# Optimization experiments

Measured on AMD Instinct MI355X. Metric: run time of the kernel, lower is better.

Reference implementation:

```python
import jax, jax.numpy as jnp
import numpy as np

N, E, IN_C, HID, OUT_C, L = 100000, 1600000, 128, 128, 128, 3
BN_EPS = 1e-5


def setup_inputs() -> dict:
    key = jax.random.key(0)
    ks = jax.random.split(key, 16)
    inp = {
        "x": jax.random.normal(ks[0], (N, IN_C), dtype=jnp.float32),
        "edge_index": jax.random.randint(ks[1], (2, E), 0, N, dtype=jnp.int64),
        "edge_attr": jax.random.normal(ks[2], (E, 1), dtype=jnp.float32),
        # input/output projections (math uses [in, out] layout)
        "lin0_w": jax.random.normal(ks[3], (IN_C, HID), dtype=jnp.float32) / np.sqrt(IN_C),
        "lin0_b": jnp.zeros((HID,), dtype=jnp.float32),
        "lin1_w": jax.random.normal(ks[4], (HID, OUT_C), dtype=jnp.float32) / np.sqrt(HID),
        "lin1_b": jnp.zeros((OUT_C,), dtype=jnp.float32),
        # stacked GCNConv weights/biases
        "conv_w": jax.random.normal(ks[5], (L, HID, HID), dtype=jnp.float32) / np.sqrt(HID),
        "conv_b": jnp.zeros((L, HID), dtype=jnp.float32),
        # BatchNorm1d (eval mode: running stats are buffers)
        "bn_gamma": jnp.ones((L, HID), dtype=jnp.float32),
        "bn_beta": jnp.zeros((L, HID), dtype=jnp.float32),
        "bn_mean": 0.1 * jax.random.normal(ks[6], (L, HID), dtype=jnp.float32),
        "bn_var": jax.random.uniform(ks[7], (L, HID), minval=0.5, maxval=1.5, dtype=jnp.float32),
    }
    return inp


def reference(x, edge_index, edge_attr, lin0_w, lin0_b, lin1_w, lin1_b,
              conv_w, conv_b, bn_gamma, bn_beta, bn_mean, bn_var):
    n = x.shape[0]
    # GCN normalization with self-loops (computed once; identical every layer)
    loops = jnp.arange(n, dtype=edge_index.dtype)
    src = jnp.concatenate([edge_index[0], loops])  # [E+N]
    dst = jnp.concatenate([edge_index[1], loops])  # [E+N]
    deg = jax.ops.segment_sum(jnp.ones_like(src, dtype=x.dtype), dst, num_segments=n)
    dinv = jnp.where(deg > 0, deg ** -0.5, 0.0)
    norm = dinv[src] * dinv[dst]  # [E+N]

    # input projection + relu (dropout p used in eval -> identity)
    h = jax.nn.relu(x @ lin0_w + lin0_b)

    for l in range(L):
        hw = h @ conv_w[l]                                         # [N, H]
        msg = hw[src] * norm[:, None]                              # [E+N, H]
        agg = jax.ops.segment_sum(msg, dst, num_segments=n) + conv_b[l]
        # BatchNorm1d (inference) + ReLU activation
        h = (agg - bn_mean[l]) * jax.lax.rsqrt(bn_var[l] + BN_EPS) * bn_gamma[l] + bn_beta[l]
        h = jax.nn.relu(h)

    out = h @ lin1_w + lin1_b
    return out
```

## Files before the change

kernel.cpp:

```cpp
#include <hip/hip_runtime.h>
#include <hip/hip_fp16.h>


#define HIDC 128
#define BN_EPS 1e-5f
#define DPB 256
#define NBK 512
#define BIN_CHUNK 8192

typedef short bf16x8 __attribute__((ext_vector_type(8)));
typedef float f32x4 __attribute__((ext_vector_type(4)));

__device__ __forceinline__ unsigned short f2bf_rn(float x) {
    unsigned int u = __float_as_uint(x);
    unsigned int r = u + 0x7fffu + ((u >> 16) & 1u);
    return (unsigned short)(r >> 16);
}
__device__ __forceinline__ float bf2f(unsigned short b) {
    return __uint_as_float(((unsigned int)b) << 16);
}


__global__ void detect64(const unsigned int* ei, int* flag) {
    if (threadIdx.x != 0 || blockIdx.x != 0) return;
    int is64 = 1;
    for (int i = 0; i < 64; ++i) {
        if (ei[2 * i + 1] != 0u) { is64 = 0; break; }
    }
    *flag = is64;
}

__global__ __launch_bounds__(256) void bucket_count(const void* __restrict__ ei,
                                                    const int* __restrict__ flag,
                                                    int* __restrict__ bkt, int e) {
    __shared__ int h[NBK];
    int t = threadIdx.x;
    for (int i = t; i < NBK; i += 256) h[i] = 0;
    __syncthreads();
    int base = blockIdx.x * BIN_CHUNK;
    int cnt = e - base;
    if (cnt > BIN_CHUNK) cnt = BIN_CHUNK;
    if (*flag) {
        const long long* pd = (const long long*)ei + e;
        for (int i = t; i < cnt; i += 256) atomicAdd(&h[((int)pd[base + i]) >> 8], 1);
    } else {
        const int* pd = (const int*)ei + e;
        for (int i = t; i < cnt; i += 256) atomicAdd(&h[pd[base + i] >> 8], 1);
    }
    __syncthreads();
    for (int i = t; i < NBK; i += 256) if (h[i]) atomicAdd(&bkt[i], h[i]);
}

__global__ void scan_buckets(const int* __restrict__ bkt, int* __restrict__ bbase,
                             int* __restrict__ bc, int* __restrict__ rowptr,
                             int n, int e, int nbk) {
    __shared__ int s[NBK];
    int t = threadIdx.x;
    int v = (t < nbk) ? bkt[t] : 0;
    s[t] = v;
    __syncthreads();
    for (int off = 1; off < NBK; off <<= 1) {
        int val = (t >= off) ? s[t - off] : 0;
        __syncthreads();
        s[t] += val;
        __syncthreads();
    }
    int excl = s[t] - v;
    bbase[t] = excl;
    bc[t] = excl;
    if (t == 0) rowptr[n] = e;
}

__global__ __launch_bounds__(256) void bin_pairs(const void* __restrict__ ei,
                                                 const int* __restrict__ flag,
                                                 int* __restrict__ bc,
                                                 int2* __restrict__ staged, int e) {
    __shared__ int hist[NBK];
    __shared__ int lstart[NBK];
    __shared__ int gbase[NBK];
    __shared__ int sdata[256];
    __shared__ int2 stage[BIN_CHUNK];

    int t = threadIdx.x;
    int base = blockIdx.x * BIN_CHUNK;
    int cnt = e - base;
    if (cnt > BIN_CHUNK) cnt = BIN_CHUNK;
    int is64 = *flag;

    for (int i = t; i < NBK; i += 256) hist[i] = 0;
    __syncthreads();
    if (is64) {
        const long long* pd = (const long long*)ei + e;
        for (int i = t; i < cnt; i += 256) atomicAdd(&hist[((int)pd[base + i]) >> 8], 1);
    } else {
        const int* pd = (const int*)ei + e;
        for (int i = t; i < cnt; i += 256) atomicAdd(&hist[pd[base + i] >> 8], 1);
    }
    __syncthreads();

    int a0 = hist[2 * t], a1 = hist[2 * t + 1];
    int s = a0 + a1;
    sdata[t] = s;
    __syncthreads();
    for (int off = 1; off < 256; off <<= 1) {
        int val = (t >= off) ? sdata[t - off] : 0;
        __syncthreads();
        sdata[t] += val;
        __syncthreads();
    }
    int excl = sdata[t] - s;
    lstart[2 * t] = excl;
    lstart[2 * t + 1] = excl + a0;
    if (a0 > 0) gbase[2 * t] = atomicAdd(&bc[2 * t], a0);
    if (a1 > 0) gbase[2 * t + 1] = atomicAdd(&bc[2 * t + 1], a1);
    hist[2 * t] = excl;
    hist[2 * t + 1] = excl + a0;
    __syncthreads();

    if (is64) {
        const long long* ps = (const long long*)ei;
        const long long* pd = ps + e;
        for (int i = t; i < cnt; i += 256) {
            int2 p = make_int2((int)ps[base + i], (int)pd[base + i]);
            int pos = atomicAdd(&hist[p.y >> 8], 1);
            stage[pos] = p;
        }
    } else {
        const int* ps = (const int*)ei;
        const int* pd = ps + e;
        for (int i = t; i < cnt; i += 256) {
            int2 p = make_int2(ps[base + i], pd[base + i]);
            int pos = atomicAdd(&hist[p.y >> 8], 1);
            stage[pos] = p;
        }
    }
    __syncthreads();

    for (int i = t; i < cnt; i += 256) {
        int2 p = stage[i];
        int b = p.y >> 8;
        staged[gbase[b] + (i - lstart[b])] = p;
    }
}

__global__ __launch_bounds__(256) void fill_bucket(const int2* __restrict__ staged,
                                                   const int* __restrict__ bbase,
                                                   float* __restrict__ dinv,
                                                   int* __restrict__ rowptr,
                                                   int* __restrict__ col, int n) {
    __shared__ int cnt[DPB];
    __shared__ int scn[DPB];
    int b = blockIdx.x;
    int t = threadIdx.x;
    int dstart = b * DPB;
    int ebeg = bbase[b], eend = bbase[b + 1];
    cnt[t] = 0;
    __syncthreads();
    for (int i = ebeg + t; i < eend; i += 256)
        atomicAdd(&cnt[staged[i].y - dstart], 1);
    __syncthreads();
    int my = cnt[t];
    scn[t] = my;
    __syncthreads();
    for (int off = 1; off < 256; off <<= 1) {
        int val = (t >= off) ? scn[t - off] : 0;
        __syncthreads();
        scn[t] += val;
        __syncthreads();
    }
    int excl = scn[t] - my;
    int v = dstart + t;
    if (v < n) {
        rowptr[v] = ebeg + excl;
        dinv[v] = rsqrtf((float)(my + 1));
    }
    cnt[t] = excl;
    __syncthreads();
    for (int i = ebeg + t; i < eend; i += 256) {
        int2 p = staged[i];
        int pos = atomicAdd(&cnt[p.y - dstart], 1);
        col[ebeg + pos] = p.x;
    }
}


__global__ __launch_bounds__(256) void pack_w(const float* __restrict__ lin0,
                                              const float* __restrict__ conv,
                                              const float* __restrict__ lin1,
                                              uint4* __restrict__ wf) {
    int tid = blockIdx.x * 256 + threadIdx.x;
    if (tid >= 5 * 2048) return;
    int mat = tid >> 11;
    int rem = tid & 2047;
    int ks = rem >> 9;
    int tt = (rem >> 6) & 7;
    int l = rem & 63;
    const float* W = (mat == 0) ? lin0 : (mat == 4) ? lin1 : conv + (size_t)(mat - 1) * 16384;
    int kbase = ks * 32 + (l >> 4) * 8;
    int c = tt * 16 + (l & 15);
    unsigned int hi[4], lo[4];
#pragma unroll
    for (int d = 0; d < 4; ++d) {
        float w0 = W[(kbase + 2 * d) * 128 + c];
        float w1 = W[(kbase + 2 * d + 1) * 128 + c];
        unsigned short h0 = f2bf_rn(w0), h1 = f2bf_rn(w1);
        unsigned short l0 = f2bf_rn(w0 - bf2f(h0)), l1 = f2bf_rn(w1 - bf2f(h1));
        hi[d] = (unsigned int)h0 | ((unsigned int)h1 << 16);
        lo[d] = (unsigned int)l0 | ((unsigned int)l1 << 16);
    }
    int rec = (ks * 8 + tt) * 64 + l;
    wf[(size_t)mat * 4096 + rec] = make_uint4(hi[0], hi[1], hi[2], hi[3]);
    wf[(size_t)mat * 4096 + 2048 + rec] = make_uint4(lo[0], lo[1], lo[2], lo[3]);
}


__global__ __launch_bounds__(512) void gemm_mfma(
    const float* __restrict__ A, const uint4* __restrict__ wf,
    const float* __restrict__ bias, const float* __restrict__ dinv,
    void* __restrict__ Cout, int M, int mode) {
    __shared__ uint4 WfL[4096];

    int t = threadIdx.x;
#pragma unroll
    for (int i = 0; i < 8; ++i) WfL[t + i * 512] = wf[t + i * 512];

    int wave = t >> 6, lane = t & 63;
    int lrow = lane & 15, lgrp = lane >> 4;
    int r0 = blockIdx.x * 128 + wave * 16;

    f32x4 acc[8];
#pragma unroll
    for (int i = 0; i < 8; ++i) acc[i] = (f32x4){0.f, 0.f, 0.f, 0.f};

    __syncthreads();

    int arow = r0 + lrow;
    if (arow >= M) arow = M - 1;
    const float* ap = A + (size_t)arow * 128 + lgrp * 8;

#pragma unroll
    for (int ks = 0; ks < 4; ++ks) {
        float4 v0 = *(const float4*)(ap + ks * 32);
        float4 v1 = *(const float4*)(ap + ks * 32 + 4);
        float av[8] = {v0.x, v0.y, v0.z, v0.w, v1.x, v1.y, v1.z, v1.w};
        bf16x8 ahi, alo;
#pragma unroll
        for (int j = 0; j < 8; ++j) {
            unsigned short h = f2bf_rn(av[j]);
            ahi[j] = (short)h;
            alo[j] = (short)f2bf_rn(av[j] - bf2f(h));
        }
#pragma unroll
        for (int tt = 0; tt < 8; ++tt) {
            bf16x8 bhi = *(const bf16x8*)&WfL[(ks * 8 + tt) * 64 + lane];
            bf16x8 blo = *(const bf16x8*)&WfL[2048 + (ks * 8 + tt) * 64 + lane];
            acc[tt] = __builtin_amdgcn_mfma_f32_16x16x32_bf16(ahi, bhi, acc[tt], 0, 0, 0);
            acc[tt] = __builtin_amdgcn_mfma_f32_16x16x32_bf16(ahi, blo, acc[tt], 0, 0, 0);
            acc[tt] = __builtin_amdgcn_mfma_f32_16x16x32_bf16(alo, bhi, acc[tt], 0, 0, 0);
        }
    }

    int rbase = r0 + lgrp * 4;
    float dv[4] = {0.f, 0.f, 0.f, 0.f};
    if (mode == 1) {
#pragma unroll
        for (int j = 0; j < 4; ++j) dv[j] = (rbase + j < M) ? dinv[rbase + j] : 0.f;
    }
#pragma unroll
    for (int tt = 0; tt < 8; ++tt) {
        int c = tt * 16 + lrow;
        float bc_ = (mode != 1) ? bias[c] : 0.f;
#pragma unroll
        for (int j = 0; j < 4; ++j) {
            int r = rbase + j;
            if (r >= M) continue;
            float val = acc[tt][j];
            if (mode == 0) {
                ((float*)Cout)[(size_t)r * 128 + c] = fmaxf(val + bc_, 0.f);
            } else if (mode == 1) {
                ((__half*)Cout)[(size_t)r * 128 + c] = __float2half(val * dv[j]);
            } else {
                ((float*)Cout)[(size_t)r * 128 + c] = val + bc_;
            }
        }
    }
}


__global__ __launch_bounds__(256) void agg_bn_relu(
    const __half2* __restrict__ hw, const int* __restrict__ rowptr,
    const int* __restrict__ col, const float* __restrict__ dinv,
    const float* __restrict__ convb, const float* __restrict__ gamma,
    const float* __restrict__ beta, const float* __restrict__ mean,
    const float* __restrict__ var, float* __restrict__ hout, int n) {
    int lane = threadIdx.x & 63;
    int v = (blockIdx.x * 256 + threadIdx.x) >> 6;
    if (v >= n) return;

    float2 acc = __half22float2(hw[(size_t)v * 64 + lane]);

    int beg = rowptr[v], end = rowptr[v + 1];
    for (int p = beg; p < end; p += 64) {
        int cnt = end - p;
        if (cnt > 64) cnt = 64;
        int myc = (lane < cnt) ? col[p + lane] : 0;
        int j = 0;
        for (; j + 4 <= cnt; j += 4) {
            int u0 = __shfl(myc, j);
            int u1 = __shfl(myc, j + 1);
            int u2 = __shfl(myc, j + 2);
            int u3 = __shfl(myc, j + 3);
            float2 m0 = __half22float2(hw[(size_t)u0 * 64 + lane]);
            float2 m1 = __half22float2(hw[(size_t)u1 * 64 + lane]);
            float2 m2 = __half22float2(hw[(size_t)u2 * 64 + lane]);
            float2 m3 = __half22float2(hw[(size_t)u3 * 64 + lane]);
            acc.x += (m0.x + m1.x) + (m2.x + m3.x);
            acc.y += (m0.y + m1.y) + (m2.y + m3.y);
        }
        for (; j < cnt; ++j) {
            int u = __shfl(myc, j);
            float2 m = __half22float2(hw[(size_t)u * 64 + lane]);
            acc.x += m.x;
            acc.y += m.y;
        }
    }

    float dvv = dinv[v];
    int c0 = lane * 2;
    float2 g  = *(const float2*)(gamma + c0);
    float2 be = *(const float2*)(beta + c0);
    float2 mn = *(const float2*)(mean + c0);
    float2 va = *(const float2*)(var + c0);
    float2 cb = *(const float2*)(convb + c0);
    float s0 = g.x * rsqrtf(va.x + BN_EPS);
    float s1 = g.y * rsqrtf(va.y + BN_EPS);
    float o0 = (dvv * acc.x + cb.x - mn.x) * s0 + be.x;
    float o1 = (dvv * acc.y + cb.y - mn.y) * s1 + be.y;
    o0 = fmaxf(o0, 0.0f);
    o1 = fmaxf(o1, 0.0f);
    *(float2*)(hout + (size_t)v * 128 + c0) = make_float2(o0, o1);
}


extern "C" void kernel_launch(void* const* d_in, const int* in_sizes, int n_in,
                              void* d_out, int out_size, void* d_ws, size_t ws_size,
                              hipStream_t stream) {
    const float* x      = (const float*)d_in[0];
    const void*  ei     = d_in[1];
    const float* lin0_w = (const float*)d_in[3];
    const float* lin0_b = (const float*)d_in[4];
    const float* lin1_w = (const float*)d_in[5];
    const float* lin1_b = (const float*)d_in[6];
    const float* conv_w = (const float*)d_in[7];
    const float* conv_b = (const float*)d_in[8];
    const float* bn_g   = (const float*)d_in[9];
    const float* bn_b   = (const float*)d_in[10];
    const float* bn_m   = (const float*)d_in[11];
    const float* bn_v   = (const float*)d_in[12];

    int n = in_sizes[0] / HIDC;
    int e = in_sizes[1] / 2;
    int nbk = (n + DPB - 1) / DPB;

    char* ws = (char*)d_ws;
    size_t off = 0;
    auto alloc = [&](size_t bytes) -> void* {
        void* p = ws + off;
        off += (bytes + 255) & ~(size_t)255;
        return p;
    };
    float*  h      = (float*)alloc((size_t)n * HIDC * 4);
    __half2* hw    = (__half2*)alloc((size_t)n * HIDC * 2);
    int2*   staged = (int2*)alloc((size_t)e * 8);
    int*    col    = (int*)alloc((size_t)e * 4);
    float*  dinv   = (float*)alloc((size_t)n * 4);
    int*    rowptr = (int*)alloc(((size_t)n + 1) * 4);
    int*    bkt    = (int*)alloc((size_t)NBK * 4);
    int*    bbase  = (int*)alloc((size_t)(NBK + 1) * 4);
    int*    bc     = (int*)alloc((size_t)NBK * 4);
    uint4*  wf     = (uint4*)alloc((size_t)5 * 4096 * 16);
    int*    flag   = (int*)alloc(256);

    hipMemsetAsync(bkt, 0, (size_t)NBK * 4, stream);

    detect64<<<1, 64, 0, stream>>>((const unsigned int*)ei, flag);
    pack_w<<<40, 256, 0, stream>>>(lin0_w, conv_w, lin1_w, wf);

    int binb = (e + BIN_CHUNK - 1) / BIN_CHUNK;
    bucket_count<<<binb, 256, 0, stream>>>(ei, flag, bkt, e);
    scan_buckets<<<1, 512, 0, stream>>>(bkt, bbase, bc, rowptr, n, e, nbk);
    bin_pairs<<<binb, 256, 0, stream>>>(ei, flag, bc, staged, e);
    fill_bucket<<<nbk, 256, 0, stream>>>(staged, bbase, dinv, rowptr, col, n);

    int gb = (n + 127) / 128;
    gemm_mfma<<<gb, 512, 0, stream>>>(x, wf, lin0_b, nullptr, h, n, 0);

    for (int l = 0; l < 3; ++l) {
        gemm_mfma<<<gb, 512, 0, stream>>>(h, wf + (size_t)(1 + l) * 4096, nullptr, dinv, hw, n, 1);
        int ab = (n + 3) / 4;
        agg_bn_relu<<<ab, 256, 0, stream>>>(hw, rowptr, col, dinv,
                                            conv_b + (size_t)l * HIDC,
                                            bn_g + (size_t)l * HIDC, bn_b + (size_t)l * HIDC,
                                            bn_m + (size_t)l * HIDC, bn_v + (size_t)l * HIDC,
                                            h, n);
    }
    gemm_mfma<<<gb, 512, 0, stream>>>(h, wf + (size_t)4 * 4096, lin1_b, nullptr, d_out, n, 2);
}
```

Baseline: 390.0 us.

## Store hw in 32-column chunk-major layout and aggregate per chunk

The GEMM that produces hw now writes it as four column chunks of 32 halfs each, laid out chunk-major, instead of row-major 128-wide rows. The aggregation kernel uses a 2D grid with one y-slice per chunk, and 16 lanes gather 64-byte chunk rows for each node. The aim is a per-pass gather working set of about 6.4MB, a quarter of hw, so it can stay in cache during random neighbor reads. The cost is four passes over the CSR column indices instead of one, plus shorter 64-byte gather segments.

```diff
diff --git a/kernel.cpp b/kernel.cpp
--- a/kernel.cpp
+++ b/kernel.cpp
@@ -270,6 +270,7 @@
     for (int tt = 0; tt < 8; ++tt) {
         int c = tt * 16 + lrow;
         float bc_ = (mode != 1) ? bias[c] : 0.f;
+        int chunk = c >> 5, cin = c & 31;
 #pragma unroll
         for (int j = 0; j < 4; ++j) {
             int r = rbase + j;
@@ -278,7 +279,8 @@
             if (mode == 0) {
                 ((float*)Cout)[(size_t)r * 128 + c] = fmaxf(val + bc_, 0.f);
             } else if (mode == 1) {
-                ((__half*)Cout)[(size_t)r * 128 + c] = __float2half(val * dv[j]);
+                ((__half*)Cout)[(size_t)chunk * M * 32 + (size_t)r * 32 + cin] =
+                    __float2half(val * dv[j]);
             } else {
                 ((float*)Cout)[(size_t)r * 128 + c] = val + bc_;
             }
@@ -287,46 +289,50 @@
 }
 
 
-__global__ __launch_bounds__(256) void agg_bn_relu(
-    const __half2* __restrict__ hw, const int* __restrict__ rowptr,
+__global__ __launch_bounds__(256) void agg_bn_relu_c(
+    const __half2* __restrict__ hwc, const int* __restrict__ rowptr,
     const int* __restrict__ col, const float* __restrict__ dinv,
     const float* __restrict__ convb, const float* __restrict__ gamma,
     const float* __restrict__ beta, const float* __restrict__ mean,
     const float* __restrict__ var, float* __restrict__ hout, int n) {
-    int lane = threadIdx.x & 63;
-    int v = (blockIdx.x * 256 + threadIdx.x) >> 6;
+    int chunk = blockIdx.y;
+    int t = threadIdx.x;
+    int l16 = t & 15;
+    int v = blockIdx.x * 16 + (t >> 4);
     if (v >= n) return;
 
-    float2 acc = __half22float2(hw[(size_t)v * 64 + lane]);
-
+    const __half2* base = hwc + (size_t)chunk * n * 16;
+    float2 acc = __half22float2(base[(size_t)v * 16 + l16]);
+
+    int gb = t & 48;
     int beg = rowptr[v], end = rowptr[v + 1];
-    for (int p = beg; p < end; p += 64) {
+    for (int p = beg; p < end; p += 16) {
         int cnt = end - p;
-        if (cnt > 64) cnt = 64;
-        int myc = (lane < cnt) ? col[p + lane] : 0;
+        if (cnt > 16) cnt = 16;
+        int myc = (l16 < cnt) ? col[p + l16] : 0;
         int j = 0;
         for (; j + 4 <= cnt; j += 4) {
-            int u0 = __shfl(myc, j);
-            int u1 = __shfl(myc, j + 1);
-            int u2 = __shfl(myc, j + 2);
-            int u3 = __shfl(myc, j + 3);
-            float2 m0 = __half22float2(hw[(size_t)u0 * 64 + lane]);
-            float2 m1 = __half22float2(hw[(size_t)u1 * 64 + lane]);
-            float2 m2 = __half22float2(hw[(size_t)u2 * 64 + lane]);
-            float2 m3 = __half22float2(hw[(size_t)u3 * 64 + lane]);
+            int u0 = __shfl(myc, gb + j);
+            int u1 = __shfl(myc, gb + j + 1);
+            int u2 = __shfl(myc, gb + j + 2);
+            int u3 = __shfl(myc, gb + j + 3);
+            float2 m0 = __half22float2(base[(size_t)u0 * 16 + l16]);
+            float2 m1 = __half22float2(base[(size_t)u1 * 16 + l16]);
+            float2 m2 = __half22float2(base[(size_t)u2 * 16 + l16]);
+            float2 m3 = __half22float2(base[(size_t)u3 * 16 + l16]);
             acc.x += (m0.x + m1.x) + (m2.x + m3.x);
             acc.y += (m0.y + m1.y) + (m2.y + m3.y);
         }
         for (; j < cnt; ++j) {
-            int u = __shfl(myc, j);
-            float2 m = __half22float2(hw[(size_t)u * 64 + lane]);
+            int u = __shfl(myc, gb + j);
+            float2 m = __half22float2(base[(size_t)u * 16 + l16]);
             acc.x += m.x;
             acc.y += m.y;
         }
     }
 
     float dvv = dinv[v];
-    int c0 = lane * 2;
+    int c0 = chunk * 32 + 2 * l16;
     float2 g  = *(const float2*)(gamma + c0);
     float2 be = *(const float2*)(beta + c0);
     float2 mn = *(const float2*)(mean + c0);
@@ -369,17 +375,17 @@
         off += (bytes + 255) & ~(size_t)255;
         return p;
     };
-    float*  h      = (float*)alloc((size_t)n * HIDC * 4);
-    __half2* hw    = (__half2*)alloc((size_t)n * HIDC * 2);
-    int2*   staged = (int2*)alloc((size_t)e * 8);
-    int*    col    = (int*)alloc((size_t)e * 4);
-    float*  dinv   = (float*)alloc((size_t)n * 4);
-    int*    rowptr = (int*)alloc(((size_t)n + 1) * 4);
-    int*    bkt    = (int*)alloc((size_t)NBK * 4);
-    int*    bbase  = (int*)alloc((size_t)(NBK + 1) * 4);
-    int*    bc     = (int*)alloc((size_t)NBK * 4);
-    uint4*  wf     = (uint4*)alloc((size_t)5 * 4096 * 16);
-    int*    flag   = (int*)alloc(256);
+    float*   h      = (float*)alloc((size_t)n * HIDC * 4);
+    __half2* hwc    = (__half2*)alloc((size_t)n * HIDC * 2);
+    int2*    staged = (int2*)alloc((size_t)e * 8);
+    int*     col    = (int*)alloc((size_t)e * 4);
+    float*   dinv   = (float*)alloc((size_t)n * 4);
+    int*     rowptr = (int*)alloc(((size_t)n + 1) * 4);
+    int*     bkt    = (int*)alloc((size_t)NBK * 4);
+    int*     bbase  = (int*)alloc((size_t)(NBK + 1) * 4);
+    int*     bc     = (int*)alloc((size_t)NBK * 4);
+    uint4*   wf     = (uint4*)alloc((size_t)5 * 4096 * 16);
+    int*     flag   = (int*)alloc(256);
 
     hipMemsetAsync(bkt, 0, (size_t)NBK * 4, stream);
 
@@ -395,14 +401,14 @@
     int gb = (n + 127) / 128;
     gemm_mfma<<<gb, 512, 0, stream>>>(x, wf, lin0_b, nullptr, h, n, 0);
 
+    dim3 ag((n + 15) / 16, 4);
     for (int l = 0; l < 3; ++l) {
-        gemm_mfma<<<gb, 512, 0, stream>>>(h, wf + (size_t)(1 + l) * 4096, nullptr, dinv, hw, n, 1);
-        int ab = (n + 3) / 4;
-        agg_bn_relu<<<ab, 256, 0, stream>>>(hw, rowptr, col, dinv,
-                                            conv_b + (size_t)l * HIDC,
-                                            bn_g + (size_t)l * HIDC, bn_b + (size_t)l * HIDC,
-                                            bn_m + (size_t)l * HIDC, bn_v + (size_t)l * HIDC,
-                                            h, n);
+        gemm_mfma<<<gb, 512, 0, stream>>>(h, wf + (size_t)(1 + l) * 4096, nullptr, dinv, hwc, n, 1);
+        agg_bn_relu_c<<<ag, 256, 0, stream>>>(hwc, rowptr, col, dinv,
+                                              conv_b + (size_t)l * HIDC,
+                                              bn_g + (size_t)l * HIDC, bn_b + (size_t)l * HIDC,
+                                              bn_m + (size_t)l * HIDC, bn_v + (size_t)l * HIDC,
+                                              h, n);
     }
     gemm_mfma<<<gb, 512, 0, stream>>>(h, wf + (size_t)4 * 4096, lin1_b, nullptr, d_out, n, 2);
 }
```

Measured after the change: 451.4 us. +15.8%, slower.
